# Optimization experiments

Measured on AMD Instinct MI355X. Metric: run time of the kernel, lower is better.

## Reference

```python
import jax, jax.numpy as jnp
import numpy as np

B, N, DEG, LOOKBACK, DIM, OUT = 256, 512, 16, 5, 64, 6
E = B * N * DEG            # 2,097,152 directed edges
NN = B * N                 # 131,072 nodes
K1 = int(np.ceil(0.8 * N))    # 410 nodes kept per graph after pool1
K2 = int(np.ceil(0.8 * K1))   # 328 nodes kept per graph after pool2


def setup_inputs():
    key = jax.random.key(0)
    ks = jax.random.split(key, 14)
    x = jax.random.normal(ks[0], (NN, LOOKBACK), jnp.float32)
    # per-graph random edges, then shift into the global node index space
    local = jax.random.randint(ks[1], (2, E), 0, N)
    offsets = jnp.repeat(jnp.arange(B, dtype=jnp.int32) * N, N * DEG)
    edge_index = local + offsets[None, :]

    def lin(k, fi, fo):
        return jax.random.normal(k, (fi, fo), jnp.float32) / np.sqrt(fi)

    return {
        "x": x,
        "edge_index": edge_index,
        "c1_Wl": lin(ks[2], LOOKBACK, DIM), "c1_bl": jnp.zeros((DIM,), jnp.float32),
        "c1_Wr": lin(ks[3], LOOKBACK, DIM),
        "pool1_w": jax.random.normal(ks[4], (DIM,), jnp.float32) / np.sqrt(DIM),
        "c2_Wl": lin(ks[5], DIM, DIM), "c2_bl": jnp.zeros((DIM,), jnp.float32),
        "c2_Wr": lin(ks[6], DIM, DIM),
        "pool2_w": jax.random.normal(ks[7], (DIM,), jnp.float32) / np.sqrt(DIM),
        "lin1_W": lin(ks[8], 2 * DIM, DIM), "lin1_b": jnp.zeros((DIM,), jnp.float32),
        "lin2_W": lin(ks[9], DIM, OUT), "lin2_b": jnp.zeros((OUT,), jnp.float32),
    }


def _sage(x, src, dst, valid, Wl, bl, Wr, n_nodes):
    # PyG SAGEConv: out = lin_l(mean_{j->i} x_j) + lin_r(x_i); empty nbhd -> 0
    msg = x[src] * valid[:, None]
    s = jax.ops.segment_sum(msg, dst, num_segments=n_nodes)
    deg = jax.ops.segment_sum(valid, dst, num_segments=n_nodes)
    mean = s / jnp.maximum(deg, 1.0)[:, None]
    return mean @ Wl + bl + x @ Wr


def _topk(x, w, nb, npg, k):
    # PyG TopKPooling: score = tanh(x.w/||w||), keep top-k per graph, scale kept rows
    score = jnp.tanh((x @ w) / jnp.linalg.norm(w))
    vals, idx = jax.lax.top_k(score.reshape(nb, npg), k)     # [nb, k]
    perm = (idx + (jnp.arange(nb) * npg)[:, None]).reshape(-1)
    return x[perm] * vals.reshape(-1, 1), perm


def _readout(x, nb, k):
    r = x.reshape(nb, k, -1)
    return jnp.concatenate([r.max(axis=1), r.mean(axis=1)], axis=1)  # [gmp | gap]


def reference(x, edge_index, c1_Wl, c1_bl, c1_Wr, pool1_w,
              c2_Wl, c2_bl, c2_Wr, pool2_w, lin1_W, lin1_b, lin2_W, lin2_b):
    src, dst = edge_index[0], edge_index[1]
    valid0 = jnp.ones((E,), jnp.float32)

    h = jax.nn.relu(_sage(x, src, dst, valid0, c1_Wl, c1_bl, c1_Wr, NN))
    h, perm1 = _topk(h, pool1_w, B, N, K1)
    x1 = _readout(h, B, K1)

    # filter_adj: remap edges to pooled node ids, mask dropped edges
    n1 = B * K1
    inv = jnp.full((NN,), -1, jnp.int32).at[perm1].set(jnp.arange(n1, dtype=jnp.int32))
    s1, d1 = inv[src], inv[dst]
    valid1 = ((s1 >= 0) & (d1 >= 0)).astype(jnp.float32)
    s1 = jnp.maximum(s1, 0)
    d1 = jnp.maximum(d1, 0)

    h = jax.nn.relu(_sage(h, s1, d1, valid1, c2_Wl, c2_bl, c2_Wr, n1))
    h, _ = _topk(h, pool2_w, B, K1, K2)
    x2 = _readout(h, B, K2)

    z = x1 + x2
    z = jax.nn.relu(z @ lin1_W + lin1_b)
    return z @ lin2_W + lin2_b
```

## Files before the change

### kernel.cpp

```cpp
#include <hip/hip_runtime.h>
#include <hip/hip_bf16.h>

#define BGR   256
#define NPG1  512
#define DEG   16
#define EPG   (NPG1 * DEG)
#define LB    5
#define DIM   64
#define OUTF  6
#define NN    (BGR * NPG1)
#define EDG   (BGR * EPG)
#define K1    410
#define K2    328
#define N1    (BGR * K1)
#define CSRW  48
#define CSRW1 56
#define GRIDW (N1 / 64)
#define GRIDA (N1 / 16)

__global__ __launch_bounds__(512)
void s1_csr_score_kernel(const float* __restrict__ x,
                         const int* __restrict__ eidx,
                         const float* __restrict__ Wl,
                         const float* __restrict__ bl,
                         const float* __restrict__ Wr,
                         const float* __restrict__ pw,
                         float* __restrict__ meanv,
                         float* __restrict__ sc1g) {
    __shared__ __align__(16) float xl[NPG1 * LB];
    __shared__ unsigned short lcsr[CSRW1 * NPG1];
    __shared__ int lcnt[NPG1];

    const int g = blockIdx.x, t = threadIdx.x;
    const int* __restrict__ src = eidx;
    const int* __restrict__ dst = eidx + EDG;

    {
        const float4* x4 = (const float4*)(x + (size_t)g * (NPG1 * LB));
        float4* xl4 = (float4*)xl;
        #pragma unroll
        for (int k = 0; k < 2; ++k) {
            int i = k * 512 + t;
            if (i < NPG1 * LB / 4) xl4[i] = x4[i];
        }
        lcnt[t] = 0;
    }
    __syncthreads();

    const int ebase = g * EPG;
    for (int k = 0; k < EPG / 512; ++k) {
        int e = ebase + k * 512 + t;
        int s = src[e] & (NPG1 - 1);
        int d = dst[e] & (NPG1 - 1);
        int slot = atomicAdd(&lcnt[d], 1);
        if (slot < CSRW1) lcsr[slot * NPG1 + d] = (unsigned short)s;
    }
    __syncthreads();

    const int dgf = lcnt[t];
    const int dg  = min(dgf, CSRW1);
    float s0 = 0.f, s1 = 0.f, s2 = 0.f, s3 = 0.f, s4 = 0.f;
    for (int k = 0; k < dg; ++k) {
        int s = lcsr[k * NPG1 + t];
        const float* xp = xl + s * LB;
        s0 += xp[0]; s1 += xp[1]; s2 += xp[2]; s3 += xp[3]; s4 += xp[4];
    }
    const float invd = 1.f / fmaxf((float)dgf, 1.f);
    float m[LB]  = { s0 * invd, s1 * invd, s2 * invd, s3 * invd, s4 * invd };
    float xv[LB];
    const int n = g * NPG1 + t;
    #pragma unroll
    for (int j = 0; j < LB; ++j) { xv[j] = xl[t * LB + j]; meanv[(size_t)n * LB + j] = m[j]; }

    const float4* Wl4 = (const float4*)Wl;
    const float4* Wr4 = (const float4*)Wr;
    const float4* bl4 = (const float4*)bl;
    const float4* pw4 = (const float4*)pw;
    float p = 0.f, q = 0.f;
    #pragma unroll 4
    for (int d4 = 0; d4 < DIM / 4; ++d4) {
        float4 bb = bl4[d4];
        float4 ww = pw4[d4];
        float4 h = bb;
        #pragma unroll
        for (int j = 0; j < LB; ++j) {
            float4 a = Wl4[j * (DIM / 4) + d4];
            float4 b = Wr4[j * (DIM / 4) + d4];
            h.x += m[j] * a.x + xv[j] * b.x;
            h.y += m[j] * a.y + xv[j] * b.y;
            h.z += m[j] * a.z + xv[j] * b.z;
            h.w += m[j] * a.w + xv[j] * b.w;
        }
        h.x = fmaxf(h.x, 0.f); h.y = fmaxf(h.y, 0.f);
        h.z = fmaxf(h.z, 0.f); h.w = fmaxf(h.w, 0.f);
        p += h.x * ww.x + h.y * ww.y + h.z * ww.z + h.w * ww.w;
        q += ww.x * ww.x + ww.y * ww.y + ww.z * ww.z + ww.w * ww.w;
    }
    sc1g[n] = tanhf(p / sqrtf(q));
}

__global__ __launch_bounds__(512)
void s1_rankpool_kernel(const float* __restrict__ x,
                        const float* __restrict__ meanv,
                        const float* __restrict__ sc1g,
                        const float* __restrict__ Wl,
                        const float* __restrict__ bl,
                        const float* __restrict__ Wr,
                        float* __restrict__ h1p,
                        int* __restrict__ invr,
                        float* __restrict__ x1buf) {
    __shared__ __align__(16) float sc[NPG1];
    __shared__ int   rnk[NPG1];
    __shared__ float redmx[8 * DIM];
    __shared__ float redsm[8 * DIM];

    const int g = blockIdx.x, t = threadIdx.x;
    const int wid = t >> 6, lane = t & 63;

    sc[t] = sc1g[g * NPG1 + t];
    __syncthreads();

    {
        float my = sc[t];
        int r = 0;
        const float4* sc4 = (const float4*)sc;
        #pragma unroll 4
        for (int j4 = 0; j4 < NPG1 / 4; ++j4) {
            float4 v = sc4[j4];
            int j = 4 * j4;
            r += (v.x > my) | ((v.x == my) & (j     < t));
            r += (v.y > my) | ((v.y == my) & (j + 1 < t));
            r += (v.z > my) | ((v.z == my) & (j + 2 < t));
            r += (v.w > my) | ((v.w == my) & (j + 3 < t));
        }
        rnk[t] = r;
        invr[g * NPG1 + t] = (r < K1) ? r : -1;
    }
    __syncthreads();

    float wlv[LB], wrv[LB];
    #pragma unroll
    for (int j = 0; j < LB; ++j) { wlv[j] = Wl[j * DIM + lane]; wrv[j] = Wr[j * DIM + lane]; }
    const float blv = bl[lane];

    float mx = -INFINITY, sm = 0.f;
    for (int n = wid; n < NPG1; n += 8) {
        int r = rnk[n];
        if (r >= K1) continue;
        const float* mp = meanv + (size_t)(g * NPG1 + n) * LB;
        const float* xp = x + (size_t)(g * NPG1 + n) * LB;
        float al = 0.f, ar = 0.f;
        #pragma unroll
        for (int j = 0; j < LB; ++j) {
            al += mp[j] * wlv[j];
            ar += xp[j] * wrv[j];
        }
        float acc = fmaxf(blv + al + ar, 0.f);
        float v = acc * sc[n];
        h1p[((size_t)g * K1 + r) * DIM + lane] = v;
        mx = fmaxf(mx, v);
        sm += v;
    }
    redmx[wid * DIM + lane] = mx;
    redsm[wid * DIM + lane] = sm;
    __syncthreads();
    if (wid == 0) {
        float m2 = redmx[lane], s2 = redsm[lane];
        #pragma unroll
        for (int w = 1; w < 8; ++w) {
            m2 = fmaxf(m2, redmx[w * DIM + lane]);
            s2 += redsm[w * DIM + lane];
        }
        x1buf[g * 2 * DIM + lane]       = m2;
        x1buf[g * 2 * DIM + DIM + lane] = s2 * (1.0f / (float)K1);
    }
}

__global__ __launch_bounds__(512)
void csr2_build_kernel(const int* __restrict__ eidx,
                       const int* __restrict__ invr,
                       unsigned short* __restrict__ csr2,
                       int* __restrict__ indeg) {
    __shared__ short linv[NPG1];
    __shared__ __align__(16) unsigned short lcsr[K1 * CSRW];
    __shared__ int lcnt[K1];

    const int g = blockIdx.x, t = threadIdx.x;
    const int* __restrict__ src = eidx;
    const int* __restrict__ dst = eidx + EDG;

    if (t < NPG1) linv[t] = (short)invr[g * NPG1 + t];
    if (t < K1) lcnt[t] = 0;
    __syncthreads();

    const int ebase = g * EPG;
    for (int k = 0; k < EPG / 512; ++k) {
        int e = ebase + k * 512 + t;
        int rs = linv[src[e] & (NPG1 - 1)];
        int rd = linv[dst[e] & (NPG1 - 1)];
        if ((rs | rd) >= 0) {
            int slot = atomicAdd(&lcnt[rd], 1);
            if (slot < CSRW) lcsr[rd * CSRW + slot] = (unsigned short)rs;
        }
    }
    __syncthreads();

    {
        const int4* ls4 = (const int4*)lcsr;
        int4* gs4 = (int4*)(csr2 + (size_t)g * K1 * CSRW);
        for (int i = t; i < K1 * CSRW / 8; i += 512) gs4[i] = ls4[i];
        if (t < K1) indeg[g * K1 + t] = min(lcnt[t], CSRW);
    }
}

__global__ __launch_bounds__(512)
void gemm2_kernel(float* __restrict__ hY,
                  float* __restrict__ Yr,
                  const float* __restrict__ Wl,
                  const float* __restrict__ bl,
                  const float* __restrict__ Wr) {
    __shared__ __align__(16) float wls[DIM * DIM];
    __shared__ __align__(16) float wrs[DIM * DIM];
    __shared__ __align__(16) float rt[64 * DIM];

    const int t = threadIdx.x, wid = t >> 6, lane = t & 63;
    const int cid = ((int)blockIdx.x & 7) * (GRIDW / 8) + ((int)blockIdx.x >> 3);
    const int nb = cid * 64;

    {
        const float4* W4l = (const float4*)Wl;
        const float4* W4r = (const float4*)Wr;
        const float4* R4  = (const float4*)&hY[(size_t)nb * DIM];
        float4* a = (float4*)wls;
        float4* b = (float4*)wrs;
        float4* r = (float4*)rt;
        #pragma unroll
        for (int k = 0; k < 2; ++k) {
            a[k * 512 + t] = W4l[k * 512 + t];
            b[k * 512 + t] = W4r[k * 512 + t];
            r[k * 512 + t] = R4[k * 512 + t];
        }
    }
    __syncthreads();

    const int r0 = wid * 8;
    float accl[8] = {0.f,0.f,0.f,0.f,0.f,0.f,0.f,0.f};
    float accr[8] = {0.f,0.f,0.f,0.f,0.f,0.f,0.f,0.f};
    #pragma unroll 4
    for (int j4 = 0; j4 < DIM / 4; ++j4) {
        const int jb = 4 * j4 * DIM + lane;
        float w0 = wls[jb],           w1 = wls[jb + DIM];
        float w2 = wls[jb + 2 * DIM], w3 = wls[jb + 3 * DIM];
        float u0 = wrs[jb],           u1 = wrs[jb + DIM];
        float u2 = wrs[jb + 2 * DIM], u3 = wrs[jb + 3 * DIM];
        #pragma unroll
        for (int i = 0; i < 8; ++i) {
            float4 a = *(const float4*)&rt[(r0 + i) * DIM + 4 * j4];
            accl[i] += a.x * w0 + a.y * w1 + a.z * w2 + a.w * w3;
            accr[i] += a.x * u0 + a.y * u1 + a.z * u2 + a.w * u3;
        }
    }
    const float bv = bl[lane];
    #pragma unroll
    for (int i = 0; i < 8; ++i) {
        hY[(size_t)(nb + r0 + i) * DIM + lane] = accl[i];
        Yr[(size_t)(nb + r0 + i) * DIM + lane] = accr[i] + bv;
    }
}

__global__ __launch_bounds__(256)
void gather2_kernel(const float* __restrict__ Yl,
                    float* __restrict__ Yh,
                    const unsigned short* __restrict__ csr2,
                    const int* __restrict__ indeg,
                    const float* __restrict__ pw,
                    float* __restrict__ sc2g) {
    const int t = threadIdx.x, wid = t >> 6, lane = t & 63;
    const int cid = ((int)blockIdx.x & 7) * (GRIDA / 8) + ((int)blockIdx.x >> 3);
    const int n0 = cid * 16 + wid * 4;

    const float pwv = pw[lane];
    float q = pwv * pwv;
    #pragma unroll
    for (int o = 32; o; o >>= 1) q += __shfl_xor(q, o);
    const float inv_nrm = 1.f / sqrtf(q);

    #pragma unroll
    for (int i = 0; i < 4; ++i) {
        const int n = n0 + i;
        const int dg = indeg[n];
        const int gb = (n / K1) * K1;
        const int4* cr = (const int4*)(csr2 + (size_t)n * CSRW);
        float acc = 0.f;
        for (int kc = 0; 8 * kc < dg; ++kc) {
            int4 wv = cr[kc];
            int k0 = 8 * kc;
            #define GACC(wrd, sh, kk)                                      \
            {   int _loc = ((wrd) >> (sh)) & 0xffff;                       \
                int _id  = ((kk) < dg) ? gb + _loc : 0;                    \
                float _v = Yl[(size_t)_id * DIM + lane];                   \
                acc += ((kk) < dg) ? _v : 0.f; }
            GACC(wv.x, 0, k0)     GACC(wv.x, 16, k0 + 1)
            GACC(wv.y, 0, k0 + 2) GACC(wv.y, 16, k0 + 3)
            GACC(wv.z, 0, k0 + 4) GACC(wv.z, 16, k0 + 5)
            GACC(wv.w, 0, k0 + 6) GACC(wv.w, 16, k0 + 7)
            #undef GACC
        }
        const float invd = 1.f / fmaxf((float)dg, 1.f);
        const float h = fmaxf(acc * invd + Yh[(size_t)n * DIM + lane], 0.f);
        Yh[(size_t)n * DIM + lane] = h;
        float p = h * pwv;
        #pragma unroll
        for (int o = 32; o; o >>= 1) p += __shfl_xor(p, o);
        if (lane == 0) sc2g[n] = tanhf(p * inv_nrm);
    }
}

__global__ __launch_bounds__(512)
void pool2_mlp_kernel(const float* __restrict__ sc2g,
                      const float* __restrict__ h2,
                      const float* __restrict__ x1buf,
                      const float* __restrict__ W1,
                      const float* __restrict__ b1,
                      const float* __restrict__ W2,
                      const float* __restrict__ b2,
                      float* __restrict__ out) {
    __shared__ __align__(16) float sc2[412];
    __shared__ int   rnk2[K1];
    __shared__ float redmx[8 * DIM];
    __shared__ float redsm[8 * DIM];
    __shared__ float zy[2 * DIM + DIM];

    const int g = blockIdx.x, t = threadIdx.x;
    const int wid = t >> 6, lane = t & 63;

    if (t < K1) sc2[t] = sc2g[g * K1 + t];
    if (t >= K1 && t < 412) sc2[t] = -INFINITY;
    __syncthreads();

    if (t < K1) {
        float my = sc2[t];
        int r = 0;
        const float4* sc4 = (const float4*)sc2;
        #pragma unroll 4
        for (int j4 = 0; j4 < 103; ++j4) {
            float4 v = sc4[j4];
            int j = 4 * j4;
            r += (v.x > my) | ((v.x == my) & (j     < t));
            r += (v.y > my) | ((v.y == my) & (j + 1 < t));
            r += (v.z > my) | ((v.z == my) & (j + 2 < t));
            r += (v.w > my) | ((v.w == my) & (j + 3 < t));
        }
        rnk2[t] = r;
    }
    __syncthreads();

    float mx = -INFINITY, sm = 0.f;
    for (int n = wid; n < K1; n += 8) {
        if (rnk2[n] < K2) {
            float v = h2[((size_t)g * K1 + n) * DIM + lane] * sc2[n];
            mx = fmaxf(mx, v);
            sm += v;
        }
    }
    redmx[wid * DIM + lane] = mx;
    redsm[wid * DIM + lane] = sm;
    __syncthreads();
    if (wid == 0) {
        float m2 = redmx[lane], s2 = redsm[lane];
        #pragma unroll
        for (int w = 1; w < 8; ++w) {
            m2 = fmaxf(m2, redmx[w * DIM + lane]);
            s2 += redsm[w * DIM + lane];
        }
        zy[lane]       = x1buf[g * 2 * DIM + lane]       + m2;
        zy[DIM + lane] = x1buf[g * 2 * DIM + DIM + lane] + s2 * (1.0f / (float)K2);
    }
    __syncthreads();

    if (t < DIM) {
        float a = b1[t];
        #pragma unroll 8
        for (int j = 0; j < 2 * DIM; ++j) a += zy[j] * W1[j * DIM + t];
        zy[2 * DIM + t] = fmaxf(a, 0.f);
    }
    __syncthreads();
    if (t < OUTF) {
        float a = b2[t];
        #pragma unroll
        for (int j = 0; j < DIM; ++j) a += zy[2 * DIM + j] * W2[j * OUTF + t];
        out[g * OUTF + t] = a;
    }
}

extern "C" void kernel_launch(void* const* d_in, const int* in_sizes, int n_in,
                              void* d_out, int out_size, void* d_ws, size_t ws_size,
                              hipStream_t stream) {
    (void)in_sizes; (void)n_in; (void)out_size; (void)ws_size;
    const float* x       = (const float*)d_in[0];
    const int*   eidx    = (const int*)d_in[1];
    const float* c1_Wl   = (const float*)d_in[2];
    const float* c1_bl   = (const float*)d_in[3];
    const float* c1_Wr   = (const float*)d_in[4];
    const float* pool1_w = (const float*)d_in[5];
    const float* c2_Wl   = (const float*)d_in[6];
    const float* c2_bl   = (const float*)d_in[7];
    const float* c2_Wr   = (const float*)d_in[8];
    const float* pool2_w = (const float*)d_in[9];
    const float* lin1_W  = (const float*)d_in[10];
    const float* lin1_b  = (const float*)d_in[11];
    const float* lin2_W  = (const float*)d_in[12];
    const float* lin2_b  = (const float*)d_in[13];
    float* out = (float*)d_out;

    char* w = (char*)d_ws;
    size_t off = 0;
    auto alloc = [&](size_t bytes) {
        void* p = w + off;
        off = (off + bytes + 255) & ~(size_t)255;
        return p;
    };
    float* h1p   = (float*)alloc((size_t)N1 * DIM * 4);
    int*   invr  = (int*)  alloc((size_t)NN * 4);
    float* x1buf = (float*)alloc((size_t)BGR * 2 * DIM * 4);
    float* sc2g  = (float*)alloc((size_t)N1 * 4);
    int*   indeg = (int*)  alloc((size_t)N1 * 4);
    float* Yh    = (float*)alloc((size_t)N1 * DIM * 4);
    char*  csreg = (char*) alloc((size_t)N1 * CSRW * 2);

    float* Yl    = h1p;
    unsigned short* csr2 = (unsigned short*)csreg;
    float* meanv = (float*)csreg;
    float* sc1g  = meanv + (size_t)NN * LB;

    s1_csr_score_kernel<<<BGR, 512, 0, stream>>>(x, eidx, c1_Wl, c1_bl, c1_Wr,
                                                 pool1_w, meanv, sc1g);
    s1_rankpool_kernel<<<BGR, 512, 0, stream>>>(x, meanv, sc1g, c1_Wl, c1_bl,
                                                c1_Wr, h1p, invr, x1buf);
    csr2_build_kernel<<<BGR, 512, 0, stream>>>(eidx, invr, csr2, indeg);
    gemm2_kernel<<<GRIDW, 512, 0, stream>>>(h1p, Yh, c2_Wl, c2_bl, c2_Wr);
    gather2_kernel<<<GRIDA, 256, 0, stream>>>(Yl, Yh, csr2, indeg, pool2_w, sc2g);
    pool2_mlp_kernel<<<BGR, 512, 0, stream>>>(sc2g, Yh, x1buf, lin1_W, lin1_b,
                                              lin2_W, lin2_b, out);
}
```

Before: 192.0 us.

## Pad per-graph rows with a zero sentinel to remove gather tail predication

Adds one zeroed padding row per graph (K1+1 rows) in the pooled feature buffers and fills unused CSR slots with the sentinel index, so the gather loop can read all 8 neighbours per chunk without per-edge bounds checks. The gather uses a per-graph base pointer, two accumulators and a scalarized node index. gemm2 now runs over the padded row count with a linear block mapping. This costs extra LDS fill work in CSR build and slightly more GEMM rows, and it reads padding entries for rows whose degree is not a multiple of 8.

```diff
diff --git a/kernel.cpp b/kernel.cpp
--- a/kernel.cpp
+++ b/kernel.cpp
@@ -13,9 +13,11 @@
 #define K1    410
 #define K2    328
 #define N1    (BGR * K1)
+#define K1P   (K1 + 1)
+#define NR    (BGR * K1P)
 #define CSRW  48
 #define CSRW1 56
-#define GRIDW (N1 / 64)
+#define GRIDW (NR / 64)
 #define GRIDA (N1 / 16)
 
 __global__ __launch_bounds__(512)
@@ -118,6 +120,7 @@
     const int wid = t >> 6, lane = t & 63;
 
     sc[t] = sc1g[g * NPG1 + t];
+    if (t < DIM) h1p[((size_t)g * K1P + K1) * DIM + t] = 0.f;
     __syncthreads();
 
     {
@@ -157,7 +160,7 @@
         }
         float acc = fmaxf(blv + al + ar, 0.f);
         float v = acc * sc[n];
-        h1p[((size_t)g * K1 + r) * DIM + lane] = v;
+        h1p[((size_t)g * K1P + r) * DIM + lane] = v;
         mx = fmaxf(mx, v);
         sm += v;
     }
@@ -191,6 +194,11 @@
 
     if (t < NPG1) linv[t] = (short)invr[g * NPG1 + t];
     if (t < K1) lcnt[t] = 0;
+    {
+        const int fill = (K1 << 16) | K1;
+        int* li = (int*)lcsr;
+        for (int i = t; i < K1 * CSRW / 2; i += 512) li[i] = fill;
+    }
     __syncthreads();
 
     const int ebase = g * EPG;
@@ -224,8 +232,7 @@
     __shared__ __align__(16) float rt[64 * DIM];
 
     const int t = threadIdx.x, wid = t >> 6, lane = t & 63;
-    const int cid = ((int)blockIdx.x & 7) * (GRIDW / 8) + ((int)blockIdx.x >> 3);
-    const int nb = cid * 64;
+    const int nb = (int)blockIdx.x * 64;
 
     {
         const float4* W4l = (const float4*)Wl;
@@ -277,7 +284,7 @@
                     float* __restrict__ sc2g) {
     const int t = threadIdx.x, wid = t >> 6, lane = t & 63;
     const int cid = ((int)blockIdx.x & 7) * (GRIDA / 8) + ((int)blockIdx.x >> 3);
-    const int n0 = cid * 16 + wid * 4;
+    const int nb = __builtin_amdgcn_readfirstlane(cid * 16 + wid * 4);
 
     const float pwv = pw[lane];
     float q = pwv * pwv;
@@ -287,28 +294,29 @@
 
     #pragma unroll
     for (int i = 0; i < 4; ++i) {
-        const int n = n0 + i;
+        const int n  = nb + i;
         const int dg = indeg[n];
-        const int gb = (n / K1) * K1;
+        const int g  = n / K1;
+        const int lr = n - g * K1;
+        const float* __restrict__ bp = Yl + (size_t)g * K1P * DIM;
         const int4* cr = (const int4*)(csr2 + (size_t)n * CSRW);
-        float acc = 0.f;
-        for (int kc = 0; 8 * kc < dg; ++kc) {
+        float a0 = 0.f, a1 = 0.f;
+        const int it = (dg + 7) >> 3;
+        for (int kc = 0; kc < it; ++kc) {
             int4 wv = cr[kc];
-            int k0 = 8 * kc;
-            #define GACC(wrd, sh, kk)                                      \
-            {   int _loc = ((wrd) >> (sh)) & 0xffff;                       \
-                int _id  = ((kk) < dg) ? gb + _loc : 0;                    \
-                float _v = Yl[(size_t)_id * DIM + lane];                   \
-                acc += ((kk) < dg) ? _v : 0.f; }
-            GACC(wv.x, 0, k0)     GACC(wv.x, 16, k0 + 1)
-            GACC(wv.y, 0, k0 + 2) GACC(wv.y, 16, k0 + 3)
-            GACC(wv.z, 0, k0 + 4) GACC(wv.z, 16, k0 + 5)
-            GACC(wv.w, 0, k0 + 6) GACC(wv.w, 16, k0 + 7)
-            #undef GACC
+            a0 += bp[((wv.x & 0xffff) << 6) + lane];
+            a1 += bp[((wv.x >> 16)    << 6) + lane];
+            a0 += bp[((wv.y & 0xffff) << 6) + lane];
+            a1 += bp[((wv.y >> 16)    << 6) + lane];
+            a0 += bp[((wv.z & 0xffff) << 6) + lane];
+            a1 += bp[((wv.z >> 16)    << 6) + lane];
+            a0 += bp[((wv.w & 0xffff) << 6) + lane];
+            a1 += bp[((wv.w >> 16)    << 6) + lane];
         }
         const float invd = 1.f / fmaxf((float)dg, 1.f);
-        const float h = fmaxf(acc * invd + Yh[(size_t)n * DIM + lane], 0.f);
-        Yh[(size_t)n * DIM + lane] = h;
+        float* yrow = Yh + (size_t)(g * K1P + lr) * DIM;
+        const float h = fmaxf((a0 + a1) * invd + yrow[lane], 0.f);
+        yrow[lane] = h;
         float p = h * pwv;
         #pragma unroll
         for (int o = 32; o; o >>= 1) p += __shfl_xor(p, o);
@@ -358,7 +366,7 @@
     float mx = -INFINITY, sm = 0.f;
     for (int n = wid; n < K1; n += 8) {
         if (rnk2[n] < K2) {
-            float v = h2[((size_t)g * K1 + n) * DIM + lane] * sc2[n];
+            float v = h2[((size_t)g * K1P + n) * DIM + lane] * sc2[n];
             mx = fmaxf(mx, v);
             sm += v;
         }
@@ -420,12 +428,12 @@
         off = (off + bytes + 255) & ~(size_t)255;
         return p;
     };
-    float* h1p   = (float*)alloc((size_t)N1 * DIM * 4);
+    float* h1p   = (float*)alloc((size_t)NR * DIM * 4);
     int*   invr  = (int*)  alloc((size_t)NN * 4);
     float* x1buf = (float*)alloc((size_t)BGR * 2 * DIM * 4);
     float* sc2g  = (float*)alloc((size_t)N1 * 4);
     int*   indeg = (int*)  alloc((size_t)N1 * 4);
-    float* Yh    = (float*)alloc((size_t)N1 * DIM * 4);
+    float* Yh    = (float*)alloc((size_t)NR * DIM * 4);
     char*  csreg = (char*) alloc((size_t)N1 * CSRW * 2);
 
     float* Yl    = h1p;
```

Result: faster. 183.5 us (-4.4%).
